# Performance work log

Hardware: AMD Instinct MI355X
Metric: run time of the kernel (lower is better)

The kernel has to match this reference:

```python
import jax, jax.numpy as jnp
import numpy as np

B, C, H, W = 32, 2, 512, 512


def setup_inputs() -> dict:
    key = jax.random.key(0)
    k1, k2 = jax.random.split(key)
    inp = jax.random.normal(k1, (B, C, H, W), dtype=jnp.float32)
    tgt = jax.random.normal(k2, (B, C, H, W), dtype=jnp.float32)
    return {"input": inp, "target": tgt}


def reference(input, target):
    b, c, h, w = input.shape
    dt = input.dtype
    # coordinate maps: (index+1)/size, kept fused via broadcasting
    x_map = jnp.arange(1, w + 1, dtype=dt) / w          # [W]
    y_map = (jnp.arange(1, h + 1, dtype=dt) / h)[:, None]  # [H,1]
    # per-(sample, channel) softmax over flattened heatmap (DSNT)
    sm = jax.nn.softmax(input.reshape(b, c, h * w), axis=-1).reshape(b, c, h, w)
    # soft-argmax coords in normalized range, then *size -> pixel coords
    pred_x = jnp.sum(sm * x_map, axis=(-2, -1)) * w     # [B,C] pixel
    pred_y = jnp.sum(sm * y_map, axis=(-2, -1)) * h     # [B,C] pixel
    # hard argmax for ground truth; ((idx % W + 1)/W)*W == idx % W + 1
    idx = jnp.argmax(target.reshape(b, c, h * w), axis=-1)  # [B,C]
    true_x = (idx % w + 1).astype(dt)                   # [B,C] pixel
    true_y = (idx // w + 1).astype(dt)                  # [B,C] pixel
    # per-point euclidean pixel distance
    ed = jnp.sqrt((true_x - pred_x) ** 2 + (true_y - pred_y) ** 2)  # [B,C]
    s_i = jnp.sum(ed[:, 0])  # channel 0: inferior
    s_s = jnp.sum(ed[:, 1])  # channel 1: superior
    # diameter (distance between the two points) difference, abs via sqrt(sq)
    pred_pts = jnp.stack([pred_x, pred_y], axis=-1)  # [B,C,2]
    true_pts = jnp.stack([true_x, true_y], axis=-1)  # [B,C,2]
    vp = pred_pts[:, 0] - pred_pts[:, 1]             # [B,2]
    vt = true_pts[:, 0] - true_pts[:, 1]             # [B,2]
    pred_dist = jnp.sqrt(jnp.sum(vp ** 2, axis=-1))
    true_dist = jnp.sqrt(jnp.sum(vt ** 2, axis=-1))
    s_diam = jnp.sum(jnp.sqrt((pred_dist - true_dist) ** 2))
    bn = jnp.asarray(b, dt)
    # coordinate lists (pixel coord - 1 as index), ordered batch-major then channel
    pred_coords = (pred_pts - 1.0).reshape(b * c, 2)
    true_coords = (true_pts - 1.0).reshape(b * c, 2)
    return (s_i / bn, s_s / bn, (s_i + s_s) / bn, s_diam / bn,
            pred_coords, true_coords)
```

## Files before the change

kernel.cpp:

```cpp
#include <hip/hip_runtime.h>
#include <math.h>

#define BATCH 32
#define CHANS 2
#define HH 512
#define WW 512
#define BC (BATCH * CHANS)
#define HMAP (HH * WW)
#define SPLITS 16
#define CHUNK (HMAP / SPLITS)
#define THREADS 256
#define V4_PER_THREAD (CHUNK / (THREADS * 4))

__global__ __launch_bounds__(THREADS)
void dsnt_partial(const float* __restrict__ inp, const float* __restrict__ tgt,
                  float* __restrict__ ps, float* __restrict__ psx,
                  float* __restrict__ psy, float* __restrict__ pmv,
                  int* __restrict__ pix) {
    const int split = blockIdx.x;
    const int bc    = blockIdx.y;
    const long base = (long)bc * HMAP + (long)split * CHUNK;
    const float4* in4 = (const float4*)(inp + base);
    const float4* tg4 = (const float4*)(tgt + base);
    const int t = threadIdx.x;

    float s = 0.f, sx = 0.f, sy = 0.f;
    float bm = -INFINITY;
    int   bi = 0;

    #pragma unroll
    for (int k = 0; k < V4_PER_THREAD; ++k) {
        const int v4 = t + k * THREADS;
        const int p  = split * CHUNK + v4 * 4;
        const float4 x = in4[v4];
        const float4 g = tg4[v4];
        const float wy  = (float)((p >> 9) + 1);
        const float wx0 = (float)((p & 511) + 1);
        const float e0 = __expf(x.x);
        const float e1 = __expf(x.y);
        const float e2 = __expf(x.z);
        const float e3 = __expf(x.w);
        const float es = (e0 + e1) + (e2 + e3);
        s  += es;
        sx += e0 * wx0 + e1 * (wx0 + 1.f) + e2 * (wx0 + 2.f) + e3 * (wx0 + 3.f);
        sy += es * wy;
        if (g.x > bm) { bm = g.x; bi = p;     }
        if (g.y > bm) { bm = g.y; bi = p + 1; }
        if (g.z > bm) { bm = g.z; bi = p + 2; }
        if (g.w > bm) { bm = g.w; bi = p + 3; }
    }

    const int lane = t & 63;
    const int wave = t >> 6;
    #pragma unroll
    for (int off = 32; off > 0; off >>= 1) {
        s  += __shfl_down(s,  off, 64);
        sx += __shfl_down(sx, off, 64);
        sy += __shfl_down(sy, off, 64);
        const float om = __shfl_down(bm, off, 64);
        const int   oi = __shfl_down(bi, off, 64);
        if (om > bm || (om == bm && oi < bi)) { bm = om; bi = oi; }
    }

    __shared__ float shs[4], shsx[4], shsy[4], shm[4];
    __shared__ int   shi[4];
    if (lane == 0) { shs[wave] = s; shsx[wave] = sx; shsy[wave] = sy;
                     shm[wave] = bm; shi[wave] = bi; }
    __syncthreads();
    if (t == 0) {
        float S = shs[0], SX = shsx[0], SY = shsy[0], M = shm[0];
        int   I = shi[0];
        #pragma unroll
        for (int w = 1; w < 4; ++w) {
            S += shs[w]; SX += shsx[w]; SY += shsy[w];
            if (shm[w] > M || (shm[w] == M && shi[w] < I)) { M = shm[w]; I = shi[w]; }
        }
        const int o = bc * SPLITS + split;
        ps[o] = S; psx[o] = SX; psy[o] = SY; pmv[o] = M; pix[o] = I;
    }
}

__global__ __launch_bounds__(64)
void dsnt_final(const float* __restrict__ ps, const float* __restrict__ psx,
                const float* __restrict__ psy, const float* __restrict__ pmv,
                const int* __restrict__ pix, float* __restrict__ out) {
    const int t = threadIdx.x;
    float S = 0.f, SX = 0.f, SY = 0.f, M = -INFINITY;
    int I = 0;
    for (int k = 0; k < SPLITS; ++k) {
        const int o = t * SPLITS + k;
        S += ps[o]; SX += psx[o]; SY += psy[o];
        const float v = pmv[o];
        const int  ix = pix[o];
        if (v > M || (v == M && ix < I)) { M = v; I = ix; }
    }
    const float px = SX / S;
    const float py = SY / S;
    const float tx = (float)((I & 511) + 1);
    const float ty = (float)((I >> 9) + 1);
    const float dx = tx - px, dy = ty - py;
    const float ed = sqrtf(dx * dx + dy * dy);

    out[4 + t * 2 + 0]   = px - 1.f;
    out[4 + t * 2 + 1]   = py - 1.f;
    out[132 + t * 2 + 0] = tx - 1.f;
    out[133 + t * 2]     = ty - 1.f;

    const float opx = __shfl_xor(px, 1, 64);
    const float opy = __shfl_xor(py, 1, 64);
    const float otx = __shfl_xor(tx, 1, 64);
    const float oty = __shfl_xor(ty, 1, 64);
    float dterm = 0.f;
    if ((t & 1) == 0) {
        const float vpx = px - opx, vpy = py - opy;
        const float vtx = tx - otx, vty = ty - oty;
        const float pd = sqrtf(vpx * vpx + vpy * vpy);
        const float td = sqrtf(vtx * vtx + vty * vty);
        dterm = fabsf(pd - td);
    }
    float e0 = ((t & 1) == 0) ? ed : 0.f;
    float e1 = ((t & 1) == 1) ? ed : 0.f;
    #pragma unroll
    for (int off = 32; off > 0; off >>= 1) {
        e0    += __shfl_down(e0, off, 64);
        e1    += __shfl_down(e1, off, 64);
        dterm += __shfl_down(dterm, off, 64);
    }
    if (t == 0) {
        const float inv = 1.0f / (float)BATCH;
        out[0] = e0 * inv;
        out[1] = e1 * inv;
        out[2] = (e0 + e1) * inv;
        out[3] = dterm * inv;
    }
}

extern "C" void kernel_launch(void* const* d_in, const int* in_sizes, int n_in,
                              void* d_out, int out_size, void* d_ws, size_t ws_size,
                              hipStream_t stream) {
    const float* inp = (const float*)d_in[0];
    const float* tgt = (const float*)d_in[1];
    float* out = (float*)d_out;

    float* ps  = (float*)d_ws;
    float* psx = ps  + BC * SPLITS;
    float* psy = psx + BC * SPLITS;
    float* pmv = psy + BC * SPLITS;
    int*   pix = (int*)(pmv + BC * SPLITS);

    dim3 grid(SPLITS, BC);
    dsnt_partial<<<grid, THREADS, 0, stream>>>(inp, tgt, ps, psx, psy, pmv, pix);
    dsnt_final<<<1, 64, 0, stream>>>(ps, psx, psy, pmv, pix, out);
}
```

Measured before the change: 148.1 us.

## Double split count, batch loads for memory-level parallelism, transpose partial layout

Doubles the per-heatmap splits to 32 so the grid has 2048 blocks, and adds an occupancy hint to launch bounds. The main loop now issues four float4 loads of input and four of target before doing any math, so more memory requests are in flight per wave. Partial results are stored split-major so the final kernel reads them coalesced across threads, and its loop is unrolled. The cost is higher register pressure from the batched loads and twice as many partials to reduce.

```diff
diff --git a/kernel.cpp b/kernel.cpp
--- a/kernel.cpp
+++ b/kernel.cpp
@@ -7,12 +7,13 @@
 #define WW 512
 #define BC (BATCH * CHANS)
 #define HMAP (HH * WW)
-#define SPLITS 16
+#define SPLITS 32
 #define CHUNK (HMAP / SPLITS)
 #define THREADS 256
 #define V4_PER_THREAD (CHUNK / (THREADS * 4))
+#define BATCH4 4
 
-__global__ __launch_bounds__(THREADS)
+__global__ __launch_bounds__(THREADS, 8)
 void dsnt_partial(const float* __restrict__ inp, const float* __restrict__ tgt,
                   float* __restrict__ ps, float* __restrict__ psx,
                   float* __restrict__ psy, float* __restrict__ pmv,
@@ -29,25 +30,33 @@
     int   bi = 0;
 
     #pragma unroll
-    for (int k = 0; k < V4_PER_THREAD; ++k) {
-        const int v4 = t + k * THREADS;
-        const int p  = split * CHUNK + v4 * 4;
-        const float4 x = in4[v4];
-        const float4 g = tg4[v4];
-        const float wy  = (float)((p >> 9) + 1);
-        const float wx0 = (float)((p & 511) + 1);
-        const float e0 = __expf(x.x);
-        const float e1 = __expf(x.y);
-        const float e2 = __expf(x.z);
-        const float e3 = __expf(x.w);
-        const float es = (e0 + e1) + (e2 + e3);
-        s  += es;
-        sx += e0 * wx0 + e1 * (wx0 + 1.f) + e2 * (wx0 + 2.f) + e3 * (wx0 + 3.f);
-        sy += es * wy;
-        if (g.x > bm) { bm = g.x; bi = p;     }
-        if (g.y > bm) { bm = g.y; bi = p + 1; }
-        if (g.z > bm) { bm = g.z; bi = p + 2; }
-        if (g.w > bm) { bm = g.w; bi = p + 3; }
+    for (int kb = 0; kb < V4_PER_THREAD / BATCH4; ++kb) {
+        float4 x[BATCH4], g[BATCH4];
+        #pragma unroll
+        for (int j = 0; j < BATCH4; ++j)
+            x[j] = in4[t + (kb * BATCH4 + j) * THREADS];
+        #pragma unroll
+        for (int j = 0; j < BATCH4; ++j)
+            g[j] = tg4[t + (kb * BATCH4 + j) * THREADS];
+        #pragma unroll
+        for (int j = 0; j < BATCH4; ++j) {
+            const int v4 = t + (kb * BATCH4 + j) * THREADS;
+            const int p  = split * CHUNK + v4 * 4;
+            const float wy  = (float)((p >> 9) + 1);
+            const float wx0 = (float)((p & 511) + 1);
+            const float e0 = __expf(x[j].x);
+            const float e1 = __expf(x[j].y);
+            const float e2 = __expf(x[j].z);
+            const float e3 = __expf(x[j].w);
+            const float es = (e0 + e1) + (e2 + e3);
+            s  += es;
+            sx += e0 * wx0 + e1 * (wx0 + 1.f) + e2 * (wx0 + 2.f) + e3 * (wx0 + 3.f);
+            sy += es * wy;
+            if (g[j].x > bm) { bm = g[j].x; bi = p;     }
+            if (g[j].y > bm) { bm = g[j].y; bi = p + 1; }
+            if (g[j].z > bm) { bm = g[j].z; bi = p + 2; }
+            if (g[j].w > bm) { bm = g[j].w; bi = p + 3; }
+        }
     }
 
     const int lane = t & 63;
@@ -75,7 +84,7 @@
             S += shs[w]; SX += shsx[w]; SY += shsy[w];
             if (shm[w] > M || (shm[w] == M && shi[w] < I)) { M = shm[w]; I = shi[w]; }
         }
-        const int o = bc * SPLITS + split;
+        const int o = split * BC + bc;
         ps[o] = S; psx[o] = SX; psy[o] = SY; pmv[o] = M; pix[o] = I;
     }
 }
@@ -87,8 +96,9 @@
     const int t = threadIdx.x;
     float S = 0.f, SX = 0.f, SY = 0.f, M = -INFINITY;
     int I = 0;
+    #pragma unroll
     for (int k = 0; k < SPLITS; ++k) {
-        const int o = t * SPLITS + k;
+        const int o = k * BC + t;
         S += ps[o]; SX += psx[o]; SY += psy[o];
         const float v = pmv[o];
         const int  ix = pix[o];
```

After: 156.3 us. 5.5% more time.

## Split heatmaps into more blocks, batch all loads upfront, parallelize final reduce

Applied to the files above, without the earlier changes.

Raises the per-heatmap split count from 16 to 64, so the grid has four times as many blocks and each thread handles four float4 pairs. All eight loads are issued before any compute to raise memory-level parallelism. The partial-result layout becomes split-major and the final kernel uses 256 threads with an LDS combine to absorb the larger partial count. The x-weighted sum is also refactored algebraically to save multiplies. The cost is more blocks and more partials written and re-read.

```diff
diff --git a/kernel.cpp b/kernel.cpp
--- a/kernel.cpp
+++ b/kernel.cpp
@@ -7,10 +7,9 @@
 #define WW 512
 #define BC (BATCH * CHANS)
 #define HMAP (HH * WW)
-#define SPLITS 16
+#define SPLITS 64
 #define CHUNK (HMAP / SPLITS)
 #define THREADS 256
-#define V4_PER_THREAD (CHUNK / (THREADS * 4))
 
 __global__ __launch_bounds__(THREADS)
 void dsnt_partial(const float* __restrict__ inp, const float* __restrict__ tgt,
@@ -24,31 +23,41 @@
     const float4* tg4 = (const float4*)(tgt + base);
     const int t = threadIdx.x;
 
+    const float4 x0 = in4[t];
+    const float4 x1 = in4[t + 1 * THREADS];
+    const float4 x2 = in4[t + 2 * THREADS];
+    const float4 x3 = in4[t + 3 * THREADS];
+    const float4 g0 = tg4[t];
+    const float4 g1 = tg4[t + 1 * THREADS];
+    const float4 g2 = tg4[t + 2 * THREADS];
+    const float4 g3 = tg4[t + 3 * THREADS];
+
     float s = 0.f, sx = 0.f, sy = 0.f;
     float bm = -INFINITY;
     int   bi = 0;
 
-    #pragma unroll
-    for (int k = 0; k < V4_PER_THREAD; ++k) {
-        const int v4 = t + k * THREADS;
-        const int p  = split * CHUNK + v4 * 4;
-        const float4 x = in4[v4];
-        const float4 g = tg4[v4];
-        const float wy  = (float)((p >> 9) + 1);
-        const float wx0 = (float)((p & 511) + 1);
-        const float e0 = __expf(x.x);
-        const float e1 = __expf(x.y);
-        const float e2 = __expf(x.z);
-        const float e3 = __expf(x.w);
-        const float es = (e0 + e1) + (e2 + e3);
-        s  += es;
-        sx += e0 * wx0 + e1 * (wx0 + 1.f) + e2 * (wx0 + 2.f) + e3 * (wx0 + 3.f);
-        sy += es * wy;
-        if (g.x > bm) { bm = g.x; bi = p;     }
-        if (g.y > bm) { bm = g.y; bi = p + 1; }
-        if (g.z > bm) { bm = g.z; bi = p + 2; }
-        if (g.w > bm) { bm = g.w; bi = p + 3; }
+#define CONSUME(X, G, J)                                                    \
+    {                                                                       \
+        const int p = split * CHUNK + (t + (J) * THREADS) * 4;              \
+        const float wy = (float)((p >> 9) + 1);                             \
+        const float wx = (float)((p & 511) + 1);                            \
+        const float e0 = __expf(X.x), e1 = __expf(X.y);                     \
+        const float e2 = __expf(X.z), e3 = __expf(X.w);                     \
+        const float es = (e0 + e1) + (e2 + e3);                             \
+        s  += es;                                                           \
+        sx += es * wx + (e1 + 2.f * e2 + 3.f * e3);                         \
+        sy += es * wy;                                                      \
+        if (G.x > bm) { bm = G.x; bi = p;     }                             \
+        if (G.y > bm) { bm = G.y; bi = p + 1; }                             \
+        if (G.z > bm) { bm = G.z; bi = p + 2; }                             \
+        if (G.w > bm) { bm = G.w; bi = p + 3; }                             \
     }
+
+    CONSUME(x0, g0, 0)
+    CONSUME(x1, g1, 1)
+    CONSUME(x2, g2, 2)
+    CONSUME(x3, g3, 3)
+#undef CONSUME
 
     const int lane = t & 63;
     const int wave = t >> 6;
@@ -75,25 +84,45 @@
             S += shs[w]; SX += shsx[w]; SY += shsy[w];
             if (shm[w] > M || (shm[w] == M && shi[w] < I)) { M = shm[w]; I = shi[w]; }
         }
-        const int o = bc * SPLITS + split;
+        const int o = split * BC + bc;
         ps[o] = S; psx[o] = SX; psy[o] = SY; pmv[o] = M; pix[o] = I;
     }
 }
 
-__global__ __launch_bounds__(64)
+__global__ __launch_bounds__(256)
 void dsnt_final(const float* __restrict__ ps, const float* __restrict__ psx,
                 const float* __restrict__ psy, const float* __restrict__ pmv,
                 const int* __restrict__ pix, float* __restrict__ out) {
-    const int t = threadIdx.x;
+    const int t    = threadIdx.x;
+    const int lane = t & 63;
+    const int wv   = t >> 6;
+
     float S = 0.f, SX = 0.f, SY = 0.f, M = -INFINITY;
     int I = 0;
-    for (int k = 0; k < SPLITS; ++k) {
-        const int o = t * SPLITS + k;
+    #pragma unroll
+    for (int k = 0; k < SPLITS / 4; ++k) {
+        const int o = (wv * (SPLITS / 4) + k) * BC + lane;
         S += ps[o]; SX += psx[o]; SY += psy[o];
         const float v = pmv[o];
         const int  ix = pix[o];
         if (v > M || (v == M && ix < I)) { M = v; I = ix; }
     }
+
+    __shared__ float lS[4][64], lSX[4][64], lSY[4][64], lM[4][64];
+    __shared__ int   lI[4][64];
+    lS[wv][lane] = S; lSX[wv][lane] = SX; lSY[wv][lane] = SY;
+    lM[wv][lane] = M; lI[wv][lane] = I;
+    __syncthreads();
+    if (wv != 0) return;
+
+    #pragma unroll
+    for (int w = 1; w < 4; ++w) {
+        S += lS[w][lane]; SX += lSX[w][lane]; SY += lSY[w][lane];
+        const float v = lM[w][lane];
+        const int  ix = lI[w][lane];
+        if (v > M || (v == M && ix < I)) { M = v; I = ix; }
+    }
+
     const float px = SX / S;
     const float py = SY / S;
     const float tx = (float)((I & 511) + 1);
@@ -101,32 +130,32 @@
     const float dx = tx - px, dy = ty - py;
     const float ed = sqrtf(dx * dx + dy * dy);
 
-    out[4 + t * 2 + 0]   = px - 1.f;
-    out[4 + t * 2 + 1]   = py - 1.f;
-    out[132 + t * 2 + 0] = tx - 1.f;
-    out[133 + t * 2]     = ty - 1.f;
+    out[4 + lane * 2 + 0]   = px - 1.f;
+    out[4 + lane * 2 + 1]   = py - 1.f;
+    out[132 + lane * 2 + 0] = tx - 1.f;
+    out[133 + lane * 2]     = ty - 1.f;
 
     const float opx = __shfl_xor(px, 1, 64);
     const float opy = __shfl_xor(py, 1, 64);
     const float otx = __shfl_xor(tx, 1, 64);
     const float oty = __shfl_xor(ty, 1, 64);
     float dterm = 0.f;
-    if ((t & 1) == 0) {
+    if ((lane & 1) == 0) {
         const float vpx = px - opx, vpy = py - opy;
         const float vtx = tx - otx, vty = ty - oty;
         const float pd = sqrtf(vpx * vpx + vpy * vpy);
         const float td = sqrtf(vtx * vtx + vty * vty);
         dterm = fabsf(pd - td);
     }
-    float e0 = ((t & 1) == 0) ? ed : 0.f;
-    float e1 = ((t & 1) == 1) ? ed : 0.f;
+    float e0 = ((lane & 1) == 0) ? ed : 0.f;
+    float e1 = ((lane & 1) == 1) ? ed : 0.f;
     #pragma unroll
     for (int off = 32; off > 0; off >>= 1) {
         e0    += __shfl_down(e0, off, 64);
         e1    += __shfl_down(e1, off, 64);
         dterm += __shfl_down(dterm, off, 64);
     }
-    if (t == 0) {
+    if (lane == 0) {
         const float inv = 1.0f / (float)BATCH;
         out[0] = e0 * inv;
         out[1] = e1 * inv;
@@ -150,5 +179,5 @@
 
     dim3 grid(SPLITS, BC);
     dsnt_partial<<<grid, THREADS, 0, stream>>>(inp, tgt, ps, psx, psy, pmv, pix);
-    dsnt_final<<<1, 64, 0, stream>>>(ps, psx, psy, pmv, pix, out);
+    dsnt_final<<<1, 256, 0, stream>>>(ps, psx, psy, pmv, pix, out);
 }
```

New measurement: 148.8 us. No clear change (+0.4%).
